# Kernel optimization log

Hardware: AMD Instinct MI355X
Metric: run time of the kernel (lower is better)

## Reference

```python
import jax, jax.numpy as jnp
import numpy as np

N, IN_DIM, KEY_DIM, K, VAL_DIM = 100000, 512, 100, 8, 64


def setup_inputs() -> dict:
    key = jax.random.key(0)
    ks = jax.random.split(key, 7)
    s = 0.02
    return {
        "x": jax.random.normal(ks[0], (N, IN_DIM), dtype=jnp.float32),
        "Wk": jax.random.normal(ks[1], (KEY_DIM, IN_DIM), dtype=jnp.float32) * s,
        "bk": jax.random.normal(ks[2], (KEY_DIM,), dtype=jnp.float32) * s,
        "Wq": jax.random.normal(ks[3], (K, KEY_DIM), dtype=jnp.float32) * s,
        "bq": jax.random.normal(ks[4], (K,), dtype=jnp.float32) * s,
        "Wv": jax.random.normal(ks[5], (VAL_DIM, IN_DIM), dtype=jnp.float32) * s,
        "bv": jax.random.normal(ks[6], (VAL_DIM,), dtype=jnp.float32) * s,
    }


def reference(x, Wk, bk, Wq, bq, Wv, bv):
    # torch.nn.Linear: y = x @ W.T + b
    key = x @ Wk.T + bk                  # [N, key_dim]
    val = x @ Wv.T + bv                  # [N, val_dim]
    que = key @ Wq.T + bq                # [N, k]
    # att_norm == 'softmax': per-sample softmax over the k groups
    w = jax.nn.softmax(que, axis=-1)     # [N, k]
    # per-sample outer product w_i^T @ val_i -> [N, k, val_dim]
    x_group = w[:, :, None] * val[:, None, :]
    return x_group
```

## Files before the change

kernel.cpp:

```cpp
#include <hip/hip_runtime.h>

#define NROWS 100000
#define IN_DIM 512

typedef __attribute__((ext_vector_type(8))) short short8;
typedef __attribute__((ext_vector_type(4))) float f32x4;

__device__ inline unsigned short f2bf(float f) {
    union { float f; unsigned u; } v; v.f = f;
    unsigned u = v.u;
    return (unsigned short)((u + 0x7FFFu + ((u >> 16) & 1u)) >> 16);
}

__global__ void qg_prepack(const float* __restrict__ Wk, const float* __restrict__ bk,
                           const float* __restrict__ Wq, const float* __restrict__ bq,
                           const float* __restrict__ Wv,
                           unsigned short* __restrict__ Bp, float* __restrict__ qb) {
    int id = blockIdx.x * 256 + threadIdx.x;
    if (id < 8) {
        float s = bq[id];
        #pragma unroll 4
        for (int j = 0; j < 100; ++j) s += Wq[id * 100 + j] * bk[j];
        qb[id] = s;
    }
    if (id >= 5120) return;
    int lane = id & 63;
    int ks = (id >> 6) & 15;
    int t = id >> 10;
    int c = t * 16 + (lane & 15);
    int kk = ks * 32 + (lane >> 4) * 8;
    short8 pk;
    #pragma unroll
    for (int e = 0; e < 8; ++e) {
        int k2 = kk + e;
        float w;
        if (c < 64) {
            w = Wv[c * IN_DIM + k2];
        } else if (c < 72) {
            float s = 0.f;
            #pragma unroll 4
            for (int j = 0; j < 100; ++j) s += Wq[(c - 64) * 100 + j] * Wk[j * IN_DIM + k2];
            w = s;
        } else {
            w = 0.f;
        }
        pk[e] = (short)f2bf(w);
    }
    ((short8*)Bp)[id] = pk;
}

#define CA0 "v48","v49","v50","v51","v52","v53","v54","v55"
#define CA1 "v56","v57","v58","v59","v60","v61","v62","v63"
#define CA2 "v64","v65","v66","v67","v68","v69","v70","v71"
#define CB0 "v72","v73","v74","v75","v76","v77","v78","v79","v80","v81","v82","v83","v84","v85","v86","v87","v88","v89","v90","v91"
#define CB1 "v92","v93","v94","v95","v96","v97","v98","v99","v100","v101","v102","v103","v104","v105","v106","v107","v108","v109","v110","v111"
#define CB2 "v112","v113","v114","v115","v116","v117","v118","v119","v120","v121","v122","v123","v124","v125","v126","v127","v128","v129","v130","v131"
#define COFF "v132","v133","v134","v135","v136","v137"
#define CACC "v140","v141","v142","v143","v144","v145","v146","v147","v148","v149","v150","v151","v152","v153","v154","v155","v156","v157","v158","v159"

#define ISSUE(AR0, AR1, B0, B1, B2, B3, B4, CLA, CLB)                          \
    asm volatile(                                                              \
        "global_load_dwordx4 " AR0 ", v132, %0 offset:0\n\t"                   \
        "global_load_dwordx4 " AR1 ", v132, %0 offset:16\n\t"                  \
        "v_add_u32 v132, 0x80, v132\n\t"                                       \
        "global_load_dwordx4 " B0 ", v133, %1 offset:0\n\t"                    \
        "v_add_u32 v133, 0x400, v133\n\t"                                      \
        "global_load_dwordx4 " B1 ", v134, %1 offset:0\n\t"                    \
        "v_add_u32 v134, 0x400, v134\n\t"                                      \
        "global_load_dwordx4 " B2 ", v135, %1 offset:0\n\t"                    \
        "v_add_u32 v135, 0x400, v135\n\t"                                      \
        "global_load_dwordx4 " B3 ", v136, %1 offset:0\n\t"                    \
        "v_add_u32 v136, 0x400, v136\n\t"                                      \
        "global_load_dwordx4 " B4 ", v137, %1 offset:0\n\t"                    \
        "v_add_u32 v137, 0x400, v137"                                          \
        :: "s"(x), "s"(Bp) : "memory", CLA, CLB, COFF)

#define ISSUE0 ISSUE("v[48:51]", "v[52:55]", "v[72:75]", "v[76:79]", "v[80:83]", "v[84:87]", "v[88:91]", CA0, CB0)
#define ISSUE1 ISSUE("v[56:59]", "v[60:63]", "v[92:95]", "v[96:99]", "v[100:103]", "v[104:107]", "v[108:111]", CA1, CB1)
#define ISSUE2 ISSUE("v[64:67]", "v[68:71]", "v[112:115]", "v[116:119]", "v[120:123]", "v[124:127]", "v[128:131]", CA2, CB2)

#define CONS(NW, A0s, A1s, A2s, A3s, AF, B0, B1, B2, B3, B4, CLA)              \
    asm volatile("s_waitcnt vmcnt(" NW ")" ::: "memory");                      \
    asm volatile(                                                              \
        "v_cvt_pk_bf16_f32 " A0s "\n\t"                                        \
        "v_cvt_pk_bf16_f32 " A1s "\n\t"                                        \
        "v_cvt_pk_bf16_f32 " A2s "\n\t"                                        \
        "v_cvt_pk_bf16_f32 " A3s "\n\t"                                        \
        "s_nop 1\n\t"                                                          \
        "v_mfma_f32_16x16x32_bf16 v[140:143], " AF ", " B0 ", v[140:143]\n\t"  \
        "v_mfma_f32_16x16x32_bf16 v[144:147], " AF ", " B1 ", v[144:147]\n\t"  \
        "v_mfma_f32_16x16x32_bf16 v[148:151], " AF ", " B2 ", v[148:151]\n\t"  \
        "v_mfma_f32_16x16x32_bf16 v[152:155], " AF ", " B3 ", v[152:155]\n\t"  \
        "v_mfma_f32_16x16x32_bf16 v[156:159], " AF ", " B4 ", v[156:159]"      \
        ::: "memory", CLA, CACC)

#define CONS0(NW) CONS(NW, "v48, v48, v49", "v49, v50, v51", "v50, v52, v53", "v51, v54, v55", \
                       "v[48:51]", "v[72:75]", "v[76:79]", "v[80:83]", "v[84:87]", "v[88:91]", CA0)
#define CONS1(NW) CONS(NW, "v56, v56, v57", "v57, v58, v59", "v58, v60, v61", "v59, v62, v63", \
                       "v[56:59]", "v[92:95]", "v[96:99]", "v[100:103]", "v[104:107]", "v[108:111]", CA1)
#define CONS2(NW) CONS(NW, "v64, v64, v65", "v65, v66, v67", "v66, v68, v69", "v67, v70, v71", \
                       "v[64:67]", "v[112:115]", "v[116:119]", "v[120:123]", "v[124:127]", "v[128:131]", CA2)

__global__ __launch_bounds__(128, 2) void qg_main(const float* __restrict__ x,
                                                  const float* __restrict__ bv,
                                                  const unsigned short* __restrict__ Bp,
                                                  const float* __restrict__ qb,
                                                  float* __restrict__ out) {
    __shared__ float vlds[2][16][68];
    __shared__ float wlds[2][16][8];
    const int tid = threadIdx.x;
    const int w = tid >> 6;
    const int lane = tid & 63;
    const int g = lane >> 4;
    const int cl = lane & 15;
    const int rowbase = (blockIdx.x * 2 + w) * 16;

    const unsigned voffA = (unsigned)((rowbase + cl) * 512 + g * 8) * 4u;
    const unsigned voffB = (unsigned)lane * 16u;

    float bvr[4];
    #pragma unroll
    for (int t = 0; t < 4; ++t) bvr[t] = bv[t * 16 + cl];
    float qbr = qb[cl & 7];
    asm volatile("s_waitcnt vmcnt(0)" ::: "memory");

    asm volatile(
        "v_mov_b32 v132, %0\n\t"
        "v_mov_b32 v133, %1\n\t"
        "v_mov_b32 v134, %2\n\t"
        "v_mov_b32 v135, %3\n\t"
        "v_mov_b32 v136, %4\n\t"
        "v_mov_b32 v137, %5"
        :: "v"(voffA), "v"(voffB), "v"(voffB + 16384u), "v"(voffB + 32768u),
           "v"(voffB + 49152u), "v"(voffB + 65536u)
        : COFF);
    asm volatile(
        "v_mov_b32 v140, 0\n\tv_mov_b32 v141, 0\n\tv_mov_b32 v142, 0\n\tv_mov_b32 v143, 0\n\t"
        "v_mov_b32 v144, 0\n\tv_mov_b32 v145, 0\n\tv_mov_b32 v146, 0\n\tv_mov_b32 v147, 0\n\t"
        "v_mov_b32 v148, 0\n\tv_mov_b32 v149, 0\n\tv_mov_b32 v150, 0\n\tv_mov_b32 v151, 0\n\t"
        "v_mov_b32 v152, 0\n\tv_mov_b32 v153, 0\n\tv_mov_b32 v154, 0\n\tv_mov_b32 v155, 0\n\t"
        "v_mov_b32 v156, 0\n\tv_mov_b32 v157, 0\n\tv_mov_b32 v158, 0\n\tv_mov_b32 v159, 0"
        ::: CACC);

    ISSUE0; ISSUE1; ISSUE2;
    CONS0("14"); ISSUE0;
    CONS1("14"); ISSUE1;
    CONS2("14"); ISSUE2;
    CONS0("14"); ISSUE0;
    CONS1("14"); ISSUE1;
    CONS2("14"); ISSUE2;
    CONS0("14"); ISSUE0;
    CONS1("14"); ISSUE1;
    CONS2("14"); ISSUE2;
    CONS0("14"); ISSUE0;
    CONS1("14"); ISSUE1;
    CONS2("14"); ISSUE2;
    CONS0("14"); ISSUE0;
    CONS1("14");
    CONS2("7");
    CONS0("0");

    asm volatile("s_nop 7\n\ts_nop 7\n\ts_nop 7");
    float ac[5][4];
    asm volatile("v_mov_b32 %0, v140" : "=v"(ac[0][0]));
    asm volatile("v_mov_b32 %0, v141" : "=v"(ac[0][1]));
    asm volatile("v_mov_b32 %0, v142" : "=v"(ac[0][2]));
    asm volatile("v_mov_b32 %0, v143" : "=v"(ac[0][3]));
    asm volatile("v_mov_b32 %0, v144" : "=v"(ac[1][0]));
    asm volatile("v_mov_b32 %0, v145" : "=v"(ac[1][1]));
    asm volatile("v_mov_b32 %0, v146" : "=v"(ac[1][2]));
    asm volatile("v_mov_b32 %0, v147" : "=v"(ac[1][3]));
    asm volatile("v_mov_b32 %0, v148" : "=v"(ac[2][0]));
    asm volatile("v_mov_b32 %0, v149" : "=v"(ac[2][1]));
    asm volatile("v_mov_b32 %0, v150" : "=v"(ac[2][2]));
    asm volatile("v_mov_b32 %0, v151" : "=v"(ac[2][3]));
    asm volatile("v_mov_b32 %0, v152" : "=v"(ac[3][0]));
    asm volatile("v_mov_b32 %0, v153" : "=v"(ac[3][1]));
    asm volatile("v_mov_b32 %0, v154" : "=v"(ac[3][2]));
    asm volatile("v_mov_b32 %0, v155" : "=v"(ac[3][3]));
    asm volatile("v_mov_b32 %0, v156" : "=v"(ac[4][0]));
    asm volatile("v_mov_b32 %0, v157" : "=v"(ac[4][1]));
    asm volatile("v_mov_b32 %0, v158" : "=v"(ac[4][2]));
    asm volatile("v_mov_b32 %0, v159" : "=v"(ac[4][3]));

    #pragma unroll
    for (int t = 0; t < 4; ++t) {
        #pragma unroll
        for (int r = 0; r < 4; ++r)
            vlds[w][g * 4 + r][t * 16 + cl] = ac[t][r] + bvr[t];
    }
    if (cl < 8) {
        #pragma unroll
        for (int r = 0; r < 4; ++r)
            wlds[w][g * 4 + r][cl] = ac[4][r] + qbr;
    }
    asm volatile("s_waitcnt lgkmcnt(0)" ::: "memory");

    if (lane < 16) {
        float q[8];
        float m = -1e30f;
        #pragma unroll
        for (int k = 0; k < 8; ++k) { q[k] = wlds[w][lane][k]; m = fmaxf(m, q[k]); }
        float ssum = 0.f;
        #pragma unroll
        for (int k = 0; k < 8; ++k) { q[k] = __expf(q[k] - m); ssum += q[k]; }
        float inv = 1.f / ssum;
        #pragma unroll
        for (int k = 0; k < 8; ++k) wlds[w][lane][k] = q[k] * inv;
    }
    asm volatile("s_waitcnt lgkmcnt(0)" ::: "memory");

    f32x4* outp = (f32x4*)out + (size_t)rowbase * 128;
    #pragma unroll
    for (int it = 0; it < 32; ++it) {
        int idx = it * 64 + lane;
        int row = idx >> 7;
        int j = idx & 127;
        float wgt = wlds[w][row][j >> 4];
        float4 vv = *(const float4*)&vlds[w][row][(j & 15) * 4];
        f32x4 o;
        o[0] = wgt * vv.x; o[1] = wgt * vv.y; o[2] = wgt * vv.z; o[3] = wgt * vv.w;
        __builtin_nontemporal_store(o, &outp[(size_t)row * 128 + j]);
    }
}

extern "C" void kernel_launch(void* const* d_in, const int* in_sizes, int n_in,
                              void* d_out, int out_size, void* d_ws, size_t ws_size,
                              hipStream_t stream) {
    const float* x  = (const float*)d_in[0];
    const float* Wk = (const float*)d_in[1];
    const float* bk = (const float*)d_in[2];
    const float* Wq = (const float*)d_in[3];
    const float* bq = (const float*)d_in[4];
    const float* Wv = (const float*)d_in[5];
    const float* bv = (const float*)d_in[6];
    float* out = (float*)d_out;

    unsigned short* Bp = (unsigned short*)d_ws;
    float* qb = (float*)((char*)d_ws + 81920);

    qg_prepack<<<20, 256, 0, stream>>>(Wk, bk, Wq, bq, Wv, Bp, qb);
    qg_main<<<3125, 128, 0, stream>>>(x, bv, Bp, qb, out);
}
```

Before: 101.8 us.

## Process two row tiles per wave, overlapping first tile's stores with second tile's MFMA loads

Each wave now handles two 16-row tiles. The second tile's x loads and MFMAs are interleaved with the output stores of the first tile, so memory writes overlap with reads and compute. Blocks grow to 4 waves and the grid shrinks to 782, with row indices clamped for the ragged tail; clamped rows write duplicate identical data. This adds code complexity and hand-tuned waitcnt values that must stay correct, and fewer blocks means less wave-level parallelism.

```diff
diff --git a/kernel.cpp b/kernel.cpp
--- a/kernel.cpp
+++ b/kernel.cpp
@@ -101,21 +101,55 @@
 #define CONS2(NW) CONS(NW, "v64, v64, v65", "v65, v66, v67", "v66, v68, v69", "v67, v70, v71", \
                        "v[64:67]", "v[112:115]", "v[116:119]", "v[120:123]", "v[124:127]", "v[128:131]", CA2)
 
-__global__ __launch_bounds__(128, 2) void qg_main(const float* __restrict__ x,
+#define ZERO_ACC                                                               \
+    asm volatile(                                                              \
+        "v_mov_b32 v140, 0\n\tv_mov_b32 v141, 0\n\tv_mov_b32 v142, 0\n\tv_mov_b32 v143, 0\n\t" \
+        "v_mov_b32 v144, 0\n\tv_mov_b32 v145, 0\n\tv_mov_b32 v146, 0\n\tv_mov_b32 v147, 0\n\t" \
+        "v_mov_b32 v148, 0\n\tv_mov_b32 v149, 0\n\tv_mov_b32 v150, 0\n\tv_mov_b32 v151, 0\n\t" \
+        "v_mov_b32 v152, 0\n\tv_mov_b32 v153, 0\n\tv_mov_b32 v154, 0\n\tv_mov_b32 v155, 0\n\t" \
+        "v_mov_b32 v156, 0\n\tv_mov_b32 v157, 0\n\tv_mov_b32 v158, 0\n\tv_mov_b32 v159, 0\n\t" \
+        "s_nop 1" ::: CACC)
+
+#define EXTRACT_ACC(ac)                                                        \
+    asm volatile("s_nop 7\n\ts_nop 7\n\ts_nop 7");                             \
+    asm volatile("v_mov_b32 %0, v140" : "=v"(ac[0][0]));                       \
+    asm volatile("v_mov_b32 %0, v141" : "=v"(ac[0][1]));                       \
+    asm volatile("v_mov_b32 %0, v142" : "=v"(ac[0][2]));                       \
+    asm volatile("v_mov_b32 %0, v143" : "=v"(ac[0][3]));                       \
+    asm volatile("v_mov_b32 %0, v144" : "=v"(ac[1][0]));                       \
+    asm volatile("v_mov_b32 %0, v145" : "=v"(ac[1][1]));                       \
+    asm volatile("v_mov_b32 %0, v146" : "=v"(ac[1][2]));                       \
+    asm volatile("v_mov_b32 %0, v147" : "=v"(ac[1][3]));                       \
+    asm volatile("v_mov_b32 %0, v148" : "=v"(ac[2][0]));                       \
+    asm volatile("v_mov_b32 %0, v149" : "=v"(ac[2][1]));                       \
+    asm volatile("v_mov_b32 %0, v150" : "=v"(ac[2][2]));                       \
+    asm volatile("v_mov_b32 %0, v151" : "=v"(ac[2][3]));                       \
+    asm volatile("v_mov_b32 %0, v152" : "=v"(ac[3][0]));                       \
+    asm volatile("v_mov_b32 %0, v153" : "=v"(ac[3][1]));                       \
+    asm volatile("v_mov_b32 %0, v154" : "=v"(ac[3][2]));                       \
+    asm volatile("v_mov_b32 %0, v155" : "=v"(ac[3][3]));                       \
+    asm volatile("v_mov_b32 %0, v156" : "=v"(ac[4][0]));                       \
+    asm volatile("v_mov_b32 %0, v157" : "=v"(ac[4][1]));                       \
+    asm volatile("v_mov_b32 %0, v158" : "=v"(ac[4][2]));                       \
+    asm volatile("v_mov_b32 %0, v159" : "=v"(ac[4][3]))
+
+__global__ __launch_bounds__(256, 2) void qg_main(const float* __restrict__ x,
                                                   const float* __restrict__ bv,
                                                   const unsigned short* __restrict__ Bp,
                                                   const float* __restrict__ qb,
                                                   float* __restrict__ out) {
-    __shared__ float vlds[2][16][68];
-    __shared__ float wlds[2][16][8];
+    __shared__ float vlds[4][16][68];
+    __shared__ float wlds[4][16][8];
     const int tid = threadIdx.x;
     const int w = tid >> 6;
     const int lane = tid & 63;
     const int g = lane >> 4;
     const int cl = lane & 15;
-    const int rowbase = (blockIdx.x * 2 + w) * 16;
-
-    const unsigned voffA = (unsigned)((rowbase + cl) * 512 + g * 8) * 4u;
+    const int rb1 = blockIdx.x * 128 + w * 16;
+    const int rb2 = rb1 + 64;
+
+    const unsigned voffA1 = (unsigned)(min(rb1 + cl, NROWS - 1) * 512 + g * 8) * 4u;
+    const unsigned voffA2 = (unsigned)(min(rb2 + cl, NROWS - 1) * 512 + g * 8) * 4u;
     const unsigned voffB = (unsigned)lane * 16u;
 
     float bvr[4];
@@ -125,63 +159,39 @@
     asm volatile("s_waitcnt vmcnt(0)" ::: "memory");
 
     asm volatile(
-        "v_mov_b32 v132, %0\n\t"
-        "v_mov_b32 v133, %1\n\t"
-        "v_mov_b32 v134, %2\n\t"
-        "v_mov_b32 v135, %3\n\t"
-        "v_mov_b32 v136, %4\n\t"
-        "v_mov_b32 v137, %5"
-        :: "v"(voffA), "v"(voffB), "v"(voffB + 16384u), "v"(voffB + 32768u),
-           "v"(voffB + 49152u), "v"(voffB + 65536u)
-        : COFF);
+        "v_mov_b32 v132, %0\n\tv_mov_b32 v133, %1\n\tv_mov_b32 v134, %2\n\t"
+        "v_mov_b32 v135, %3\n\tv_mov_b32 v136, %4\n\tv_mov_b32 v137, %5"
+        :: "v"(voffA1), "v"(voffB), "v"(voffB + 16384u), "v"(voffB + 32768u),
+           "v"(voffB + 49152u), "v"(voffB + 65536u) : COFF);
+    ZERO_ACC;
+
+    ISSUE0; ISSUE1; ISSUE2;
+    CONS0("14"); ISSUE0;
+    CONS1("14"); ISSUE1;
+    CONS2("14"); ISSUE2;
+    CONS0("14"); ISSUE0;
+    CONS1("14"); ISSUE1;
+    CONS2("14"); ISSUE2;
+    CONS0("14"); ISSUE0;
+    CONS1("14"); ISSUE1;
+    CONS2("14"); ISSUE2;
+    CONS0("14"); ISSUE0;
+    CONS1("14"); ISSUE1;
+    CONS2("14"); ISSUE2;
+    CONS0("14"); ISSUE0;
+    CONS1("14");
     asm volatile(
-        "v_mov_b32 v140, 0\n\tv_mov_b32 v141, 0\n\tv_mov_b32 v142, 0\n\tv_mov_b32 v143, 0\n\t"
-        "v_mov_b32 v144, 0\n\tv_mov_b32 v145, 0\n\tv_mov_b32 v146, 0\n\tv_mov_b32 v147, 0\n\t"
-        "v_mov_b32 v148, 0\n\tv_mov_b32 v149, 0\n\tv_mov_b32 v150, 0\n\tv_mov_b32 v151, 0\n\t"
-        "v_mov_b32 v152, 0\n\tv_mov_b32 v153, 0\n\tv_mov_b32 v154, 0\n\tv_mov_b32 v155, 0\n\t"
-        "v_mov_b32 v156, 0\n\tv_mov_b32 v157, 0\n\tv_mov_b32 v158, 0\n\tv_mov_b32 v159, 0"
-        ::: CACC);
-
-    ISSUE0; ISSUE1; ISSUE2;
-    CONS0("14"); ISSUE0;
-    CONS1("14"); ISSUE1;
-    CONS2("14"); ISSUE2;
-    CONS0("14"); ISSUE0;
-    CONS1("14"); ISSUE1;
-    CONS2("14"); ISSUE2;
-    CONS0("14"); ISSUE0;
-    CONS1("14"); ISSUE1;
-    CONS2("14"); ISSUE2;
-    CONS0("14"); ISSUE0;
-    CONS1("14"); ISSUE1;
-    CONS2("14"); ISSUE2;
-    CONS0("14"); ISSUE0;
-    CONS1("14");
-    CONS2("7");
-    CONS0("0");
-
-    asm volatile("s_nop 7\n\ts_nop 7\n\ts_nop 7");
+        "v_mov_b32 v132, %0\n\tv_mov_b32 v133, %1\n\tv_mov_b32 v134, %2\n\t"
+        "v_mov_b32 v135, %3\n\tv_mov_b32 v136, %4\n\tv_mov_b32 v137, %5"
+        :: "v"(voffA2), "v"(voffB), "v"(voffB + 16384u), "v"(voffB + 32768u),
+           "v"(voffB + 49152u), "v"(voffB + 65536u) : COFF);
+    ISSUE1;
+    CONS2("14"); ISSUE2;
+    CONS0("14"); ISSUE0;
+
     float ac[5][4];
-    asm volatile("v_mov_b32 %0, v140" : "=v"(ac[0][0]));
-    asm volatile("v_mov_b32 %0, v141" : "=v"(ac[0][1]));
-    asm volatile("v_mov_b32 %0, v142" : "=v"(ac[0][2]));
-    asm volatile("v_mov_b32 %0, v143" : "=v"(ac[0][3]));
-    asm volatile("v_mov_b32 %0, v144" : "=v"(ac[1][0]));
-    asm volatile("v_mov_b32 %0, v145" : "=v"(ac[1][1]));
-    asm volatile("v_mov_b32 %0, v146" : "=v"(ac[1][2]));
-    asm volatile("v_mov_b32 %0, v147" : "=v"(ac[1][3]));
-    asm volatile("v_mov_b32 %0, v148" : "=v"(ac[2][0]));
-    asm volatile("v_mov_b32 %0, v149" : "=v"(ac[2][1]));
-    asm volatile("v_mov_b32 %0, v150" : "=v"(ac[2][2]));
-    asm volatile("v_mov_b32 %0, v151" : "=v"(ac[2][3]));
-    asm volatile("v_mov_b32 %0, v152" : "=v"(ac[3][0]));
-    asm volatile("v_mov_b32 %0, v153" : "=v"(ac[3][1]));
-    asm volatile("v_mov_b32 %0, v154" : "=v"(ac[3][2]));
-    asm volatile("v_mov_b32 %0, v155" : "=v"(ac[3][3]));
-    asm volatile("v_mov_b32 %0, v156" : "=v"(ac[4][0]));
-    asm volatile("v_mov_b32 %0, v157" : "=v"(ac[4][1]));
-    asm volatile("v_mov_b32 %0, v158" : "=v"(ac[4][2]));
-    asm volatile("v_mov_b32 %0, v159" : "=v"(ac[4][3]));
+    EXTRACT_ACC(ac);
+    ZERO_ACC;
 
     #pragma unroll
     for (int t = 0; t < 4; ++t) {
@@ -195,7 +205,6 @@
             wlds[w][g * 4 + r][cl] = ac[4][r] + qbr;
     }
     asm volatile("s_waitcnt lgkmcnt(0)" ::: "memory");
-
     if (lane < 16) {
         float q[8];
         float m = -1e30f;
@@ -210,17 +219,81 @@
     }
     asm volatile("s_waitcnt lgkmcnt(0)" ::: "memory");
 
-    f32x4* outp = (f32x4*)out + (size_t)rowbase * 128;
+#define STORE2(S) do {                                                         \
+        int srow_ = min(rb1 + (S), NROWS - 1);                                 \
+        float wgt0_ = wlds[w][S][lane >> 4];                                   \
+        float wgt1_ = wlds[w][S][4 + (lane >> 4)];                             \
+        float4 vv_ = *(const float4*)&vlds[w][S][(lane & 15) * 4];             \
+        f32x4 o0_, o1_;                                                        \
+        o0_[0] = wgt0_ * vv_.x; o0_[1] = wgt0_ * vv_.y;                        \
+        o0_[2] = wgt0_ * vv_.z; o0_[3] = wgt0_ * vv_.w;                        \
+        o1_[0] = wgt1_ * vv_.x; o1_[1] = wgt1_ * vv_.y;                        \
+        o1_[2] = wgt1_ * vv_.z; o1_[3] = wgt1_ * vv_.w;                        \
+        unsigned off0_ = (unsigned)srow_ * 2048u + (unsigned)lane * 16u;       \
+        asm volatile("global_store_dwordx4 %0, %1, %2 nt"                      \
+                     :: "v"(off0_), "v"(o0_), "s"(out) : "memory");            \
+        asm volatile("global_store_dwordx4 %0, %1, %2 offset:1024 nt"          \
+                     :: "v"(off0_), "v"(o1_), "s"(out) : "memory");            \
+    } while (0)
+
+    STORE2(0);  CONS1("16"); ISSUE1;
+    STORE2(1);  CONS2("18"); ISSUE2;
+    STORE2(2);  CONS0("20"); ISSUE0;
+    STORE2(3);  CONS1("20"); ISSUE1;
+    STORE2(4);  CONS2("20"); ISSUE2;
+    STORE2(5);  CONS0("20"); ISSUE0;
+    STORE2(6);  CONS1("20"); ISSUE1;
+    STORE2(7);  CONS2("20"); ISSUE2;
+    STORE2(8);  CONS0("20"); ISSUE0;
+    STORE2(9);  CONS1("20"); ISSUE1;
+    STORE2(10); CONS2("20"); ISSUE2;
+    STORE2(11); CONS0("20"); ISSUE0;
+    STORE2(12); CONS1("20"); ISSUE1;
+    STORE2(13); CONS2("20");
+    STORE2(14); CONS0("13");
+    STORE2(15); CONS1("6");
+#undef STORE2
+
+    EXTRACT_ACC(ac);
+
+    #pragma unroll
+    for (int t = 0; t < 4; ++t) {
+        #pragma unroll
+        for (int r = 0; r < 4; ++r)
+            vlds[w][g * 4 + r][t * 16 + cl] = ac[t][r] + bvr[t];
+    }
+    if (cl < 8) {
+        #pragma unroll
+        for (int r = 0; r < 4; ++r)
+            wlds[w][g * 4 + r][cl] = ac[4][r] + qbr;
+    }
+    asm volatile("s_waitcnt lgkmcnt(0)" ::: "memory");
+    if (lane < 16) {
+        float q[8];
+        float m = -1e30f;
+        #pragma unroll
+        for (int k = 0; k < 8; ++k) { q[k] = wlds[w][lane][k]; m = fmaxf(m, q[k]); }
+        float ssum = 0.f;
+        #pragma unroll
+        for (int k = 0; k < 8; ++k) { q[k] = __expf(q[k] - m); ssum += q[k]; }
+        float inv = 1.f / ssum;
+        #pragma unroll
+        for (int k = 0; k < 8; ++k) wlds[w][lane][k] = q[k] * inv;
+    }
+    asm volatile("s_waitcnt lgkmcnt(0)" ::: "memory");
+
+    f32x4* outp = (f32x4*)out;
     #pragma unroll
     for (int it = 0; it < 32; ++it) {
         int idx = it * 64 + lane;
         int row = idx >> 7;
         int j = idx & 127;
+        int srow = min(rb2 + row, NROWS - 1);
         float wgt = wlds[w][row][j >> 4];
         float4 vv = *(const float4*)&vlds[w][row][(j & 15) * 4];
         f32x4 o;
         o[0] = wgt * vv.x; o[1] = wgt * vv.y; o[2] = wgt * vv.z; o[3] = wgt * vv.w;
-        __builtin_nontemporal_store(o, &outp[(size_t)row * 128 + j]);
+        __builtin_nontemporal_store(o, &outp[(size_t)srow * 128 + j]);
     }
 }
 
@@ -240,5 +313,5 @@
     float* qb = (float*)((char*)d_ws + 81920);
 
     qg_prepack<<<20, 256, 0, stream>>>(Wk, bk, Wq, bq, Wv, Bp, qb);
-    qg_main<<<3125, 128, 0, stream>>>(x, bv, Bp, qb, out);
+    qg_main<<<782, 256, 0, stream>>>(x, bv, Bp, qb, out);
 }
```

New measurement: 105.9 us. 4.0% more time.
